# Kernel optimization log

Hardware: AMD Instinct MI355X
Metric: run time of the kernel (lower is better)

## Reference

```python
import jax, jax.numpy as jnp
import numpy as np

N = 100000      # nodes
E = 1600000     # edges (avg degree 16)
D_IN, D_H, D_OUT = 128, 128, 64


def _pow(d, e):
    # torch code zeroes out inf from 0 ** negative_exponent
    p = jnp.power(d, e)
    return jnp.where(jnp.isinf(p), jnp.zeros_like(p), p)


def _gso_weights(params, deg, row, col):
    # params = [m1, m2, m3, e1, e2, e3, a]
    m1, m2, m3, e1, e2, e3, a = (params[i] for i in range(7))
    d = deg + a                       # self-loop-adjusted degrees, [N]
    pe2 = _pow(d, e2)
    pe3 = _pow(d, e3)
    w_edge = m2 * pe2[row] * pe3[col]                     # off-diagonal GSO entries, [E]
    w_self = m1 * _pow(d, e1) + m2 * pe2 * pe3 + m3       # diagonal GSO entries, [N]
    return w_edge, w_self


def setup_inputs() -> dict:
    key = jax.random.key(0)
    ks = jax.random.split(key, 8)
    x = jax.random.normal(ks[0], (N, D_IN), dtype=jnp.float32)
    edge_index = jax.random.randint(ks[1], (2, E), 0, N, dtype=jnp.int32)
    glorot = lambda k, i, o: jax.random.normal(k, (i, o), dtype=jnp.float32) * np.float32(np.sqrt(2.0 / (i + o)))
    W1 = glorot(ks[2], D_IN, D_H)
    W2 = glorot(ks[3], D_H, D_H)
    W3 = glorot(ks[4], D_H, D_OUT)
    b1 = jnp.zeros((D_H,), jnp.float32)
    b2 = jnp.zeros((D_H,), jnp.float32)
    b3 = jnp.zeros((D_OUT,), jnp.float32)
    # [m1, m2, m3, e1, e2, e3, a]
    gso1_params = jnp.array([0.0, 1.0, 0.0, 0.0, -0.5, -0.5, 1.0], jnp.float32)   # NORMADJ
    gso2_params = jnp.array([0.0, -1.0, 1.0, 0.0, -1.0, 0.0, 0.0], jnp.float32)   # RWLAPLACIAN
    return {"x": x, "edge_index": edge_index, "W1": W1, "b1": b1, "W2": W2,
            "b2": b2, "W3": W3, "b3": b3, "gso1_params": gso1_params,
            "gso2_params": gso2_params}


def reference(x, edge_index, W1, b1, W2, b2, W3, b3, gso1_params, gso2_params):
    row, col = edge_index[0], edge_index[1]
    deg = jax.ops.segment_sum(jnp.ones(row.shape, x.dtype), row, num_segments=N)
    we1, ws1 = _gso_weights(gso1_params, deg, row, col)
    we2, ws2 = _gso_weights(gso2_params, deg, row, col)
    w_edge = we1 + we2   # combined two-GSO edge weights, [E]
    w_self = ws1 + ws2   # combined diagonal (self-loop) weights, [N]

    def conv(h, W, b):
        h = h @ W                                                        # [N, d_out]
        agg = jax.ops.segment_sum(w_edge[:, None] * h[col], row, num_segments=N)
        return agg + w_self[:, None] * h + b

    h = jax.nn.relu(conv(x, W1, b1))
    h = jax.nn.relu(conv(h, W2, b2))   # dropout=0.0 (eval) -> identity
    return conv(h, W3, b3)
```

## Files before the change

### kernel.cpp

```cpp
#include <hip/hip_runtime.h>
#include <hip/hip_fp16.h>
#include <math.h>
#include <type_traits>

typedef _Float16 half8 __attribute__((ext_vector_type(8)));
typedef float floatx4 __attribute__((ext_vector_type(4)));

__global__ void deg_count_kernel(const int* __restrict__ row, int* __restrict__ degi, int E) {
    int g = blockIdx.x * blockDim.x + threadIdx.x;
    if (g < E) atomicAdd(&degi[row[g]], 1);
}

__device__ __forceinline__ float pow_z(float d, float e) {
    float p = powf(d, e);
    return isinf(p) ? 0.0f : p;
}

__device__ __forceinline__ void gso_coeff(float deg, const float* __restrict__ p1,
                                          const float* __restrict__ p2,
                                          float4* cf, float* ws) {
    float m1a = p1[0], m2a = p1[1], m3a = p1[2], e1a = p1[3], e2a = p1[4], e3a = p1[5], aa = p1[6];
    float m1b = p2[0], m2b = p2[1], m3b = p2[2], e1b = p2[3], e2b = p2[4], e3b = p2[5], ab = p2[6];
    float d1 = deg + aa, d2 = deg + ab;
    float pa1 = pow_z(d1, e1a), pa2 = pow_z(d1, e2a), pa3 = pow_z(d1, e3a);
    float pb1 = pow_z(d2, e1b), pb2 = pow_z(d2, e2b), pb3 = pow_z(d2, e3b);
    *cf = make_float4(m2a * pa2, pa3, m2b * pb2, pb3);
    *ws = m1a * pa1 + m2a * pa2 * pa3 + m3a
        + m1b * pb1 + m2b * pb2 * pb3 + m3b;
}

__global__ void scan_block_kernel(const int* __restrict__ degi, int* __restrict__ rowptr,
                                  int* __restrict__ blocksum,
                                  const float* __restrict__ p1, const float* __restrict__ p2,
                                  float4* __restrict__ coeff, float* __restrict__ wself, int n) {
    __shared__ int sums[256];
    int tid = threadIdx.x;
    int base = blockIdx.x * 1024 + tid * 4;
    int d0 = (base + 0 < n) ? degi[base + 0] : 0;
    int d1 = (base + 1 < n) ? degi[base + 1] : 0;
    int d2 = (base + 2 < n) ? degi[base + 2] : 0;
    int d3 = (base + 3 < n) ? degi[base + 3] : 0;
    int s0 = d0, s1 = s0 + d1, s2 = s1 + d2, s3 = s2 + d3;
    sums[tid] = s3;
    __syncthreads();
    for (int off = 1; off < 256; off <<= 1) {
        int v = (tid >= off) ? sums[tid - off] : 0;
        __syncthreads();
        sums[tid] += v;
        __syncthreads();
    }
    int excl = sums[tid] - s3;
    if (base + 0 < n) rowptr[base + 1] = excl + s0;
    if (base + 1 < n) rowptr[base + 2] = excl + s1;
    if (base + 2 < n) rowptr[base + 3] = excl + s2;
    if (base + 3 < n) rowptr[base + 4] = excl + s3;
    if (tid == 255) blocksum[blockIdx.x] = sums[255];
    int dd[4] = {d0, d1, d2, d3};
#pragma unroll
    for (int u = 0; u < 4; ++u) {
        if (base + u < n) {
            float4 cf; float ws;
            gso_coeff((float)dd[u], p1, p2, &cf, &ws);
            coeff[base + u] = cf;
            wself[base + u] = ws;
        }
    }
}

__global__ void scan_tops_kernel(const int* __restrict__ blocksum, int* __restrict__ blockoff, int nb) {
    __shared__ int s[128];
    int tid = threadIdx.x;
    int v = (tid < nb) ? blocksum[tid] : 0;
    s[tid] = v;
    __syncthreads();
    for (int off = 1; off < 128; off <<= 1) {
        int u = (tid >= off) ? s[tid - off] : 0;
        __syncthreads();
        s[tid] += u;
        __syncthreads();
    }
    if (tid < nb) blockoff[tid] = s[tid] - v;
}

__global__ void scan_add_kernel(int* __restrict__ rowptr, const int* __restrict__ blockoff, int n) {
    int g = blockIdx.x * blockDim.x + threadIdx.x;
    if (g == 0) rowptr[0] = 0;
    if (g < n) rowptr[g + 1] += blockoff[g >> 10];
}

__global__ __launch_bounds__(256) void partition_kernel(
        const int* __restrict__ row, const int* __restrict__ col,
        const int* __restrict__ rowptr, int* __restrict__ gcur,
        const float4* __restrict__ coeff, int2* __restrict__ epack_mid,
        int E, int shift, int NB) {
    __shared__ int scnt[256], sofs[256], scur[256], gslot[256];
    __shared__ int2 sdata[4096];
    __shared__ unsigned short sbkt[4096];

    int tid = threadIdx.x;
    int base = blockIdx.x * 4096;
    scnt[tid] = 0;
    __syncthreads();

    int epk[16]; float ew[16]; int eb[16];
#pragma unroll
    for (int u = 0; u < 16; ++u) {
        int e = base + u * 256 + tid;
        eb[u] = -1;
        if (e < E) {
            int r = row[e], c = col[e];
            int b = r >> shift;
            eb[u] = b;
            atomicAdd(&scnt[b], 1);
            float4 cr = coeff[r], cc = coeff[c];
            ew[u] = cr.x * cc.y + cr.z * cc.w;
            epk[u] = c | ((r & ((1 << shift) - 1)) << 20);
        }
    }
    __syncthreads();
    sofs[tid] = scnt[tid];
    __syncthreads();
    for (int off = 1; off < 256; off <<= 1) {
        int v = (tid >= off) ? sofs[tid - off] : 0;
        __syncthreads();
        sofs[tid] += v;
        __syncthreads();
    }
    int excl = sofs[tid] - scnt[tid];
    sofs[tid] = excl;
    scur[tid] = excl;
    if (tid < NB && scnt[tid] > 0)
        gslot[tid] = rowptr[tid << shift] + atomicAdd(&gcur[tid], scnt[tid]);
    __syncthreads();
#pragma unroll
    for (int u = 0; u < 16; ++u) {
        if (eb[u] >= 0) {
            int idx = atomicAdd(&scur[eb[u]], 1);
            sdata[idx] = make_int2(epk[u], __float_as_int(ew[u]));
            sbkt[idx] = (unsigned short)eb[u];
        }
    }
    __syncthreads();
    int cntR = min(4096, E - base);
    for (int i = tid; i < cntR; i += 256) {
        int b = sbkt[i];
        epack_mid[gslot[b] + (i - sofs[b])] = sdata[i];
    }
}

__global__ __launch_bounds__(256) void bucket_sort_kernel(
        const int* __restrict__ rowptr, const int2* __restrict__ epack_mid,
        int2* __restrict__ epack, int N, int shift) {
    __shared__ int lcur[4096];
    int b = blockIdx.x;
    int tid = threadIdx.x;
    int rows = 1 << shift;
    int row0 = b << shift;
    for (int j = tid; j < rows; j += 256) {
        int rid = row0 + j;
        if (rid < N) lcur[j] = rowptr[rid];
    }
    __syncthreads();
    int slice0 = rowptr[row0];
    int slice1 = rowptr[min(row0 + rows, N)];
    for (int i = slice0 + tid; i < slice1; i += 256) {
        int2 p = epack_mid[i];
        int rl = ((unsigned)p.x) >> 20;
        int pos = atomicAdd(&lcur[rl], 1);
        epack[pos] = make_int2(p.x & 0xFFFFF, p.y);
    }
}

__global__ void convert_w_all(const float* __restrict__ W1, const float* __restrict__ W2,
                              const float* __restrict__ W3, _Float16* __restrict__ Wt1,
                              _Float16* __restrict__ Wt2, _Float16* __restrict__ Wt3) {
    int g = blockIdx.x * blockDim.x + threadIdx.x;
    if (g < 16384) {
        int k = g >> 7, n = g & 127;
        Wt1[n * 128 + k] = (_Float16)W1[g];
    } else if (g < 32768) {
        int h = g - 16384; int k = h >> 7, n = h & 127;
        Wt2[n * 128 + k] = (_Float16)W2[h];
    } else if (g < 40960) {
        int h = g - 32768; int k = h >> 6, n = h & 63;
        Wt3[n * 128 + k] = (_Float16)W3[h];
    }
}

template<int TN, typename AT>
__global__ __launch_bounds__(256) void gemm_mfma(const AT* __restrict__ A,
        const _Float16* __restrict__ Wt,
        _Float16* __restrict__ C, int n) {
    constexpr int K = 128;
    constexpr int TM = 64;
    constexpr int LDK = K + 8;
    __shared__ _Float16 As[TM][LDK];
    __shared__ _Float16 Bs[TN][LDK];

    int tid = threadIdx.x;
    int wave = tid >> 6, lane = tid & 63;
    int q = lane >> 4, t = lane & 15;
    int rowbase = blockIdx.x * TM;

    if constexpr (std::is_same<AT, float>::value) {
        for (int i = tid; i < TM * K / 4; i += 256) {
            int r = i >> 5;
            int kc = (i & 31) * 4;
            int rr = rowbase + r;
            float4 v = make_float4(0.f, 0.f, 0.f, 0.f);
            if (rr < n) v = *(const float4*)&A[(size_t)rr * K + kc];
            As[r][kc + 0] = (_Float16)v.x;
            As[r][kc + 1] = (_Float16)v.y;
            As[r][kc + 2] = (_Float16)v.z;
            As[r][kc + 3] = (_Float16)v.w;
        }
    } else {
        for (int i = tid; i < TM * K / 8; i += 256) {
            int r = i >> 4;
            int kc = (i & 15) * 8;
            int rr = rowbase + r;
            uint4 v = make_uint4(0u, 0u, 0u, 0u);
            if (rr < n) v = *(const uint4*)&A[(size_t)rr * K + kc];
            *(uint4*)&As[r][kc] = v;
        }
    }
    for (int i = tid; i < TN * K / 8; i += 256) {
        int nr = i >> 4;
        int kc = (i & 15) * 8;
        *(uint4*)&Bs[nr][kc] = *(const uint4*)&Wt[(size_t)nr * K + kc];
    }
    __syncthreads();

    int m0 = wave * 16;
    floatx4 acc[TN / 16];
#pragma unroll
    for (int nt = 0; nt < TN / 16; ++nt) acc[nt] = (floatx4){0.f, 0.f, 0.f, 0.f};

#pragma unroll
    for (int kk = 0; kk < K; kk += 32) {
        half8 a = *(const half8*)&As[m0 + t][kk + q * 8];
#pragma unroll
        for (int nt = 0; nt < TN / 16; ++nt) {
            half8 b = *(const half8*)&Bs[nt * 16 + t][kk + q * 8];
            acc[nt] = __builtin_amdgcn_mfma_f32_16x16x32_f16(a, b, acc[nt], 0, 0, 0);
        }
    }

#pragma unroll
    for (int nt = 0; nt < TN / 16; ++nt) {
#pragma unroll
        for (int r = 0; r < 4; ++r) {
            int rr = rowbase + m0 + q * 4 + r;
            if (rr < n) C[(size_t)rr * TN + nt * 16 + t] = (_Float16)acc[nt][r];
        }
    }
}

__global__ __launch_bounds__(256) void agg128_kernel(const __half2* __restrict__ H,
        const int* __restrict__ rowptr, const int2* __restrict__ epack,
        const float* __restrict__ wself, const float* __restrict__ bias,
        __half2* __restrict__ out, int n) {
    int node = blockIdx.x * 4 + (threadIdx.x >> 6);
    if (node >= n) return;
    int lane = threadIdx.x & 63;
    int start = rowptr[node], end = rowptr[node + 1];
    float ws = wself[node];
    float2 hs = __half22float2(H[(size_t)node * 64 + lane]);
    float ax = ws * hs.x, ay = ws * hs.y;
    int e = start;
    for (; e + 8 <= end; e += 8) {
        int2 p0 = epack[e + 0], p1 = epack[e + 1], p2 = epack[e + 2], p3 = epack[e + 3];
        int2 p4 = epack[e + 4], p5 = epack[e + 5], p6 = epack[e + 6], p7 = epack[e + 7];
        __half2 h0 = H[(size_t)p0.x * 64 + lane];
        __half2 h1 = H[(size_t)p1.x * 64 + lane];
        __half2 h2 = H[(size_t)p2.x * 64 + lane];
        __half2 h3 = H[(size_t)p3.x * 64 + lane];
        __half2 h4 = H[(size_t)p4.x * 64 + lane];
        __half2 h5 = H[(size_t)p5.x * 64 + lane];
        __half2 h6 = H[(size_t)p6.x * 64 + lane];
        __half2 h7 = H[(size_t)p7.x * 64 + lane];
        float2 f0 = __half22float2(h0), f1 = __half22float2(h1);
        float2 f2 = __half22float2(h2), f3 = __half22float2(h3);
        float2 f4 = __half22float2(h4), f5 = __half22float2(h5);
        float2 f6 = __half22float2(h6), f7 = __half22float2(h7);
        float w0 = __int_as_float(p0.y), w1 = __int_as_float(p1.y);
        float w2 = __int_as_float(p2.y), w3 = __int_as_float(p3.y);
        float w4 = __int_as_float(p4.y), w5 = __int_as_float(p5.y);
        float w6 = __int_as_float(p6.y), w7 = __int_as_float(p7.y);
        ax += w0 * f0.x + w1 * f1.x + w2 * f2.x + w3 * f3.x
            + w4 * f4.x + w5 * f5.x + w6 * f6.x + w7 * f7.x;
        ay += w0 * f0.y + w1 * f1.y + w2 * f2.y + w3 * f3.y
            + w4 * f4.y + w5 * f5.y + w6 * f6.y + w7 * f7.y;
    }
    for (; e < end; ++e) {
        int2 pe = epack[e];
        float w = __int_as_float(pe.y);
        float2 f = __half22float2(H[(size_t)pe.x * 64 + lane]);
        ax += w * f.x; ay += w * f.y;
    }
    float2 b = *(const float2*)&bias[2 * lane];
    float vx = fmaxf(ax + b.x, 0.0f);
    float vy = fmaxf(ay + b.y, 0.0f);
    out[(size_t)node * 64 + lane] = __floats2half2_rn(vx, vy);
}

__global__ __launch_bounds__(256) void agg64_kernel(const __half* __restrict__ H,
        const int* __restrict__ rowptr, const int2* __restrict__ epack,
        const float* __restrict__ wself, const float* __restrict__ bias,
        float* __restrict__ out, int n) {
    int node = blockIdx.x * 4 + (threadIdx.x >> 6);
    if (node >= n) return;
    int lane = threadIdx.x & 63;
    int start = rowptr[node], end = rowptr[node + 1];
    float ws = wself[node];
    float acc = ws * __half2float(H[(size_t)node * 64 + lane]);
    int e = start;
    for (; e + 8 <= end; e += 8) {
        int2 p0 = epack[e + 0], p1 = epack[e + 1], p2 = epack[e + 2], p3 = epack[e + 3];
        int2 p4 = epack[e + 4], p5 = epack[e + 5], p6 = epack[e + 6], p7 = epack[e + 7];
        float f0 = __half2float(H[(size_t)p0.x * 64 + lane]);
        float f1 = __half2float(H[(size_t)p1.x * 64 + lane]);
        float f2 = __half2float(H[(size_t)p2.x * 64 + lane]);
        float f3 = __half2float(H[(size_t)p3.x * 64 + lane]);
        float f4 = __half2float(H[(size_t)p4.x * 64 + lane]);
        float f5 = __half2float(H[(size_t)p5.x * 64 + lane]);
        float f6 = __half2float(H[(size_t)p6.x * 64 + lane]);
        float f7 = __half2float(H[(size_t)p7.x * 64 + lane]);
        acc += __int_as_float(p0.y) * f0 + __int_as_float(p1.y) * f1
             + __int_as_float(p2.y) * f2 + __int_as_float(p3.y) * f3
             + __int_as_float(p4.y) * f4 + __int_as_float(p5.y) * f5
             + __int_as_float(p6.y) * f6 + __int_as_float(p7.y) * f7;
    }
    for (; e < end; ++e) {
        int2 pe = epack[e];
        acc += __int_as_float(pe.y) * __half2float(H[(size_t)pe.x * 64 + lane]);
    }
    out[(size_t)node * 64 + lane] = acc + bias[lane];
}

extern "C" void kernel_launch(void* const* d_in, const int* in_sizes, int n_in,
                              void* d_out, int out_size, void* d_ws, size_t ws_size,
                              hipStream_t stream) {
    const float* x  = (const float*)d_in[0];
    const int*   ei = (const int*)d_in[1];
    const float* W1 = (const float*)d_in[2];
    const float* b1 = (const float*)d_in[3];
    const float* W2 = (const float*)d_in[4];
    const float* b2 = (const float*)d_in[5];
    const float* W3 = (const float*)d_in[6];
    const float* b3 = (const float*)d_in[7];
    const float* p1 = (const float*)d_in[8];
    const float* p2 = (const float*)d_in[9];

    const int N = in_sizes[0] / 128;
    const int E = in_sizes[1] / 2;
    const int* row = ei;
    const int* col = ei + E;

    int shift = 0;
    while ((((N - 1) >> shift) + 1) > 256) shift++;
    const int NB = ((N - 1) >> shift) + 1;

    char* p = (char*)d_ws;
    auto alloc = [&](size_t bytes) -> void* {
        void* q = (void*)p;
        p += (bytes + 255) & ~(size_t)255;
        return q;
    };
    int*      degi      = (int*)alloc((size_t)N * 4);
    int*      gcur      = (int*)alloc(256 * 4);
    int*      rowptr    = (int*)alloc((size_t)(N + 1) * 4);
    const int NBLK      = (N + 1023) / 1024;
    int*      blocksum  = (int*)alloc((size_t)NBLK * 4);
    int*      blockoff  = (int*)alloc((size_t)NBLK * 4);
    float4*   coeff     = (float4*)alloc((size_t)N * 16);
    float*    wself     = (float*)alloc((size_t)N * 4);
    int2*     epack_mid = (int2*)alloc((size_t)E * 8);
    int2*     epack     = (int2*)alloc((size_t)E * 8);
    _Float16* Wt1       = (_Float16*)alloc(128 * 128 * 2);
    _Float16* Wt2       = (_Float16*)alloc(128 * 128 * 2);
    _Float16* Wt3       = (_Float16*)alloc(128 * 64 * 2);
    _Float16* bufH      = (_Float16*)alloc((size_t)N * 128 * 2);
    _Float16* actH      = (_Float16*)alloc((size_t)N * 128 * 2);
    (void)ws_size; (void)n_in;

    size_t zero_bytes = (size_t)((char*)rowptr - (char*)degi);
    hipMemsetAsync(degi, 0, zero_bytes, stream);

    convert_w_all<<<160, 256, 0, stream>>>(W1, W2, W3, Wt1, Wt2, Wt3);

    deg_count_kernel<<<(E + 255) / 256, 256, 0, stream>>>(row, degi, E);
    scan_block_kernel<<<NBLK, 256, 0, stream>>>(degi, rowptr, blocksum, p1, p2, coeff, wself, N);
    scan_tops_kernel<<<1, 128, 0, stream>>>(blocksum, blockoff, NBLK);
    scan_add_kernel<<<(N + 255) / 256, 256, 0, stream>>>(rowptr, blockoff, N);
    partition_kernel<<<(E + 4095) / 4096, 256, 0, stream>>>(row, col, rowptr, gcur, coeff,
                                                            epack_mid, E, shift, NB);
    bucket_sort_kernel<<<NB, 256, 0, stream>>>(rowptr, epack_mid, epack, N, shift);

    float* out = (float*)d_out;
    int aggGrid = (N + 3) / 4;
    int gemmGrid = (N + 63) / 64;
    gemm_mfma<128, float><<<gemmGrid, 256, 0, stream>>>(x, Wt1, bufH, N);
    agg128_kernel<<<aggGrid, 256, 0, stream>>>((const __half2*)bufH, rowptr, epack, wself,
                                               b1, (__half2*)actH, N);
    gemm_mfma<128, _Float16><<<gemmGrid, 256, 0, stream>>>(actH, Wt2, bufH, N);
    agg128_kernel<<<aggGrid, 256, 0, stream>>>((const __half2*)bufH, rowptr, epack, wself,
                                               b2, (__half2*)actH, N);
    gemm_mfma<64, _Float16><<<gemmGrid, 256, 0, stream>>>(actH, Wt3, bufH, N);
    agg64_kernel<<<aggGrid, 256, 0, stream>>>((const __half*)bufH, rowptr, epack, wself,
                                              b3, out, N);
}
```

Baseline: 507.2 us.

## Sort edges by row and column chunk, aggregate eight nodes per wave chunk-synchronously

```diff
diff --git a/kernel.cpp b/kernel.cpp
--- a/kernel.cpp
+++ b/kernel.cpp
@@ -6,9 +6,13 @@
 typedef _Float16 half8 __attribute__((ext_vector_type(8)));
 typedef float floatx4 __attribute__((ext_vector_type(4)));
 
-__global__ void deg_count_kernel(const int* __restrict__ row, int* __restrict__ degi, int E) {
+#define CC 16
+#define RSHIFT 9
+
+__global__ void deg_count_kernel(const int* __restrict__ row, const int* __restrict__ col,
+                                 int* __restrict__ degi2, int E, int cshift) {
     int g = blockIdx.x * blockDim.x + threadIdx.x;
-    if (g < E) atomicAdd(&degi[row[g]], 1);
+    if (g < E) atomicAdd(&degi2[row[g] * CC + (col[g] >> cshift)], 1);
 }
 
 __device__ __forceinline__ float pow_z(float d, float e) {
@@ -16,23 +20,24 @@
     return isinf(p) ? 0.0f : p;
 }
 
-__device__ __forceinline__ void gso_coeff(float deg, const float* __restrict__ p1,
-                                          const float* __restrict__ p2,
-                                          float4* cf, float* ws) {
+__global__ void node_coeff_kernel(const int* __restrict__ rowptr2,
+                                  const float* __restrict__ p1, const float* __restrict__ p2,
+                                  float4* __restrict__ coeff, float* __restrict__ wself, int N) {
+    int g = blockIdx.x * blockDim.x + threadIdx.x;
+    if (g >= N) return;
+    float deg = (float)(rowptr2[(size_t)(g + 1) * CC] - rowptr2[(size_t)g * CC]);
     float m1a = p1[0], m2a = p1[1], m3a = p1[2], e1a = p1[3], e2a = p1[4], e3a = p1[5], aa = p1[6];
     float m1b = p2[0], m2b = p2[1], m3b = p2[2], e1b = p2[3], e2b = p2[4], e3b = p2[5], ab = p2[6];
     float d1 = deg + aa, d2 = deg + ab;
     float pa1 = pow_z(d1, e1a), pa2 = pow_z(d1, e2a), pa3 = pow_z(d1, e3a);
     float pb1 = pow_z(d2, e1b), pb2 = pow_z(d2, e2b), pb3 = pow_z(d2, e3b);
-    *cf = make_float4(m2a * pa2, pa3, m2b * pb2, pb3);
-    *ws = m1a * pa1 + m2a * pa2 * pa3 + m3a
-        + m1b * pb1 + m2b * pb2 * pb3 + m3b;
+    coeff[g] = make_float4(m2a * pa2, pa3, m2b * pb2, pb3);
+    wself[g] = m1a * pa1 + m2a * pa2 * pa3 + m3a
+             + m1b * pb1 + m2b * pb2 * pb3 + m3b;
 }
 
 __global__ void scan_block_kernel(const int* __restrict__ degi, int* __restrict__ rowptr,
-                                  int* __restrict__ blocksum,
-                                  const float* __restrict__ p1, const float* __restrict__ p2,
-                                  float4* __restrict__ coeff, float* __restrict__ wself, int n) {
+                                  int* __restrict__ blocksum, int n) {
     __shared__ int sums[256];
     int tid = threadIdx.x;
     int base = blockIdx.x * 1024 + tid * 4;
@@ -55,31 +60,33 @@
     if (base + 2 < n) rowptr[base + 3] = excl + s2;
     if (base + 3 < n) rowptr[base + 4] = excl + s3;
     if (tid == 255) blocksum[blockIdx.x] = sums[255];
-    int dd[4] = {d0, d1, d2, d3};
-#pragma unroll
-    for (int u = 0; u < 4; ++u) {
-        if (base + u < n) {
-            float4 cf; float ws;
-            gso_coeff((float)dd[u], p1, p2, &cf, &ws);
-            coeff[base + u] = cf;
-            wself[base + u] = ws;
-        }
-    }
 }
 
 __global__ void scan_tops_kernel(const int* __restrict__ blocksum, int* __restrict__ blockoff, int nb) {
-    __shared__ int s[128];
+    __shared__ int s[256];
     int tid = threadIdx.x;
-    int v = (tid < nb) ? blocksum[tid] : 0;
-    s[tid] = v;
-    __syncthreads();
-    for (int off = 1; off < 128; off <<= 1) {
-        int u = (tid >= off) ? s[tid - off] : 0;
-        __syncthreads();
-        s[tid] += u;
-        __syncthreads();
-    }
-    if (tid < nb) blockoff[tid] = s[tid] - v;
+    int loc[8]; int tot = 0;
+#pragma unroll
+    for (int u = 0; u < 8; ++u) {
+        int i = tid * 8 + u;
+        loc[u] = (i < nb) ? blocksum[i] : 0;
+        tot += loc[u];
+    }
+    s[tid] = tot;
+    __syncthreads();
+    for (int off = 1; off < 256; off <<= 1) {
+        int v = (tid >= off) ? s[tid - off] : 0;
+        __syncthreads();
+        s[tid] += v;
+        __syncthreads();
+    }
+    int excl = s[tid] - tot;
+#pragma unroll
+    for (int u = 0; u < 8; ++u) {
+        int i = tid * 8 + u;
+        if (i < nb) blockoff[i] = excl;
+        excl += loc[u];
+    }
 }
 
 __global__ void scan_add_kernel(int* __restrict__ rowptr, const int* __restrict__ blockoff, int n) {
@@ -90,9 +97,9 @@
 
 __global__ __launch_bounds__(256) void partition_kernel(
         const int* __restrict__ row, const int* __restrict__ col,
-        const int* __restrict__ rowptr, int* __restrict__ gcur,
+        const int* __restrict__ rowptr2, int* __restrict__ gcur,
         const float4* __restrict__ coeff, int2* __restrict__ epack_mid,
-        int E, int shift, int NB) {
+        int E, int NB) {
     __shared__ int scnt[256], sofs[256], scur[256], gslot[256];
     __shared__ int2 sdata[4096];
     __shared__ unsigned short sbkt[4096];
@@ -109,12 +116,12 @@
         eb[u] = -1;
         if (e < E) {
             int r = row[e], c = col[e];
-            int b = r >> shift;
+            int b = r >> RSHIFT;
             eb[u] = b;
             atomicAdd(&scnt[b], 1);
             float4 cr = coeff[r], cc = coeff[c];
             ew[u] = cr.x * cc.y + cr.z * cc.w;
-            epk[u] = c | ((r & ((1 << shift) - 1)) << 20);
+            epk[u] = c | ((r & ((1 << RSHIFT) - 1)) << 20);
         }
     }
     __syncthreads();
@@ -130,7 +137,7 @@
     sofs[tid] = excl;
     scur[tid] = excl;
     if (tid < NB && scnt[tid] > 0)
-        gslot[tid] = rowptr[tid << shift] + atomicAdd(&gcur[tid], scnt[tid]);
+        gslot[tid] = rowptr2[(size_t)(tid << RSHIFT) * CC] + atomicAdd(&gcur[tid], scnt[tid]);
     __syncthreads();
 #pragma unroll
     for (int u = 0; u < 16; ++u) {
@@ -149,25 +156,26 @@
 }
 
 __global__ __launch_bounds__(256) void bucket_sort_kernel(
-        const int* __restrict__ rowptr, const int2* __restrict__ epack_mid,
-        int2* __restrict__ epack, int N, int shift) {
-    __shared__ int lcur[4096];
+        const int* __restrict__ rowptr2, const int2* __restrict__ epack_mid,
+        int2* __restrict__ epack, int N, int cshift) {
+    __shared__ int lcur[(1 << RSHIFT) * CC];
     int b = blockIdx.x;
     int tid = threadIdx.x;
-    int rows = 1 << shift;
-    int row0 = b << shift;
-    for (int j = tid; j < rows; j += 256) {
-        int rid = row0 + j;
-        if (rid < N) lcur[j] = rowptr[rid];
-    }
-    __syncthreads();
-    int slice0 = rowptr[row0];
-    int slice1 = rowptr[min(row0 + rows, N)];
+    int rows = 1 << RSHIFT;
+    int row0 = b << RSHIFT;
+    int nslots = (min(rows, N - row0)) * CC;
+    for (int j = tid; j < nslots; j += 256)
+        lcur[j] = rowptr2[(size_t)row0 * CC + j];
+    __syncthreads();
+    int slice0 = rowptr2[(size_t)row0 * CC];
+    int slice1 = rowptr2[(size_t)min(row0 + rows, N) * CC];
     for (int i = slice0 + tid; i < slice1; i += 256) {
         int2 p = epack_mid[i];
+        int colv = p.x & 0xFFFFF;
         int rl = ((unsigned)p.x) >> 20;
-        int pos = atomicAdd(&lcur[rl], 1);
-        epack[pos] = make_int2(p.x & 0xFFFFF, p.y);
+        int ch = colv >> cshift;
+        int pos = atomicAdd(&lcur[rl * CC + ch], 1);
+        epack[pos] = make_int2(colv, p.y);
     }
 }
 
@@ -189,8 +197,7 @@
 
 template<int TN, typename AT>
 __global__ __launch_bounds__(256) void gemm_mfma(const AT* __restrict__ A,
-        const _Float16* __restrict__ Wt,
-        _Float16* __restrict__ C, int n) {
+        const _Float16* __restrict__ Wt, _Float16* __restrict__ C, int n) {
     constexpr int K = 128;
     constexpr int TM = 64;
     constexpr int LDK = K + 8;
@@ -257,85 +264,114 @@
 }
 
 __global__ __launch_bounds__(256) void agg128_kernel(const __half2* __restrict__ H,
-        const int* __restrict__ rowptr, const int2* __restrict__ epack,
+        const int* __restrict__ rowptr2, const int2* __restrict__ epack,
         const float* __restrict__ wself, const float* __restrict__ bias,
-        __half2* __restrict__ out, int n) {
-    int node = blockIdx.x * 4 + (threadIdx.x >> 6);
-    if (node >= n) return;
-    int lane = threadIdx.x & 63;
-    int start = rowptr[node], end = rowptr[node + 1];
-    float ws = wself[node];
-    float2 hs = __half22float2(H[(size_t)node * 64 + lane]);
-    float ax = ws * hs.x, ay = ws * hs.y;
-    int e = start;
-    for (; e + 8 <= end; e += 8) {
-        int2 p0 = epack[e + 0], p1 = epack[e + 1], p2 = epack[e + 2], p3 = epack[e + 3];
-        int2 p4 = epack[e + 4], p5 = epack[e + 5], p6 = epack[e + 6], p7 = epack[e + 7];
-        __half2 h0 = H[(size_t)p0.x * 64 + lane];
-        __half2 h1 = H[(size_t)p1.x * 64 + lane];
-        __half2 h2 = H[(size_t)p2.x * 64 + lane];
-        __half2 h3 = H[(size_t)p3.x * 64 + lane];
-        __half2 h4 = H[(size_t)p4.x * 64 + lane];
-        __half2 h5 = H[(size_t)p5.x * 64 + lane];
-        __half2 h6 = H[(size_t)p6.x * 64 + lane];
-        __half2 h7 = H[(size_t)p7.x * 64 + lane];
-        float2 f0 = __half22float2(h0), f1 = __half22float2(h1);
-        float2 f2 = __half22float2(h2), f3 = __half22float2(h3);
-        float2 f4 = __half22float2(h4), f5 = __half22float2(h5);
-        float2 f6 = __half22float2(h6), f7 = __half22float2(h7);
-        float w0 = __int_as_float(p0.y), w1 = __int_as_float(p1.y);
-        float w2 = __int_as_float(p2.y), w3 = __int_as_float(p3.y);
-        float w4 = __int_as_float(p4.y), w5 = __int_as_float(p5.y);
-        float w6 = __int_as_float(p6.y), w7 = __int_as_float(p7.y);
-        ax += w0 * f0.x + w1 * f1.x + w2 * f2.x + w3 * f3.x
-            + w4 * f4.x + w5 * f5.x + w6 * f6.x + w7 * f7.x;
-        ay += w0 * f0.y + w1 * f1.y + w2 * f2.y + w3 * f3.y
-            + w4 * f4.y + w5 * f5.y + w6 * f6.y + w7 * f7.y;
-    }
-    for (; e < end; ++e) {
-        int2 pe = epack[e];
-        float w = __int_as_float(pe.y);
-        float2 f = __half22float2(H[(size_t)pe.x * 64 + lane]);
-        ax += w * f.x; ay += w * f.y;
+        __half2* __restrict__ out, int n, int nchunk) {
+    int wave = threadIdx.x >> 6, lane = threadIdx.x & 63;
+    int node0 = blockIdx.x * 32 + wave * 8;
+    if (node0 >= n) return;
+    int nv = min(8, n - node0);
+    float ax[8], ay[8];
+#pragma unroll
+    for (int i = 0; i < 8; ++i) { ax[i] = 0.f; ay[i] = 0.f; }
+#pragma unroll
+    for (int i = 0; i < 8; ++i) {
+        if (i < nv) {
+            float w = wself[node0 + i];
+            float2 h = __half22float2(H[(size_t)(node0 + i) * 64 + lane]);
+            ax[i] = w * h.x; ay[i] = w * h.y;
+        }
+    }
+    for (int c = 0; c < nchunk; ++c) {
+        int sa[8], ea[8];
+#pragma unroll
+        for (int i = 0; i < 8; ++i) {
+            sa[i] = (i < nv) ? rowptr2[(size_t)(node0 + i) * CC + c] : 0;
+            ea[i] = (i < nv) ? rowptr2[(size_t)(node0 + i) * CC + c + 1] : 0;
+        }
+        for (;;) {
+            bool any = false;
+            int2 pk[8];
+#pragma unroll
+            for (int i = 0; i < 8; ++i) {
+                if (sa[i] < ea[i]) { pk[i] = epack[sa[i]]; any = true; }
+            }
+            if (!any) break;
+            __half2 hh[8];
+#pragma unroll
+            for (int i = 0; i < 8; ++i)
+                if (sa[i] < ea[i]) hh[i] = H[(size_t)pk[i].x * 64 + lane];
+#pragma unroll
+            for (int i = 0; i < 8; ++i) {
+                if (sa[i] < ea[i]) {
+                    float w = __int_as_float(pk[i].y);
+                    float2 f = __half22float2(hh[i]);
+                    ax[i] += w * f.x; ay[i] += w * f.y;
+                    sa[i]++;
+                }
+            }
+        }
     }
     float2 b = *(const float2*)&bias[2 * lane];
-    float vx = fmaxf(ax + b.x, 0.0f);
-    float vy = fmaxf(ay + b.y, 0.0f);
-    out[(size_t)node * 64 + lane] = __floats2half2_rn(vx, vy);
+#pragma unroll
+    for (int i = 0; i < 8; ++i) {
+        if (i < nv) {
+            float vx = fmaxf(ax[i] + b.x, 0.f);
+            float vy = fmaxf(ay[i] + b.y, 0.f);
+            out[(size_t)(node0 + i) * 64 + lane] = __floats2half2_rn(vx, vy);
+        }
+    }
 }
 
 __global__ __launch_bounds__(256) void agg64_kernel(const __half* __restrict__ H,
-        const int* __restrict__ rowptr, const int2* __restrict__ epack,
+        const int* __restrict__ rowptr2, const int2* __restrict__ epack,
         const float* __restrict__ wself, const float* __restrict__ bias,
-        float* __restrict__ out, int n) {
-    int node = blockIdx.x * 4 + (threadIdx.x >> 6);
-    if (node >= n) return;
-    int lane = threadIdx.x & 63;
-    int start = rowptr[node], end = rowptr[node + 1];
-    float ws = wself[node];
-    float acc = ws * __half2float(H[(size_t)node * 64 + lane]);
-    int e = start;
-    for (; e + 8 <= end; e += 8) {
-        int2 p0 = epack[e + 0], p1 = epack[e + 1], p2 = epack[e + 2], p3 = epack[e + 3];
-        int2 p4 = epack[e + 4], p5 = epack[e + 5], p6 = epack[e + 6], p7 = epack[e + 7];
-        float f0 = __half2float(H[(size_t)p0.x * 64 + lane]);
-        float f1 = __half2float(H[(size_t)p1.x * 64 + lane]);
-        float f2 = __half2float(H[(size_t)p2.x * 64 + lane]);
-        float f3 = __half2float(H[(size_t)p3.x * 64 + lane]);
-        float f4 = __half2float(H[(size_t)p4.x * 64 + lane]);
-        float f5 = __half2float(H[(size_t)p5.x * 64 + lane]);
-        float f6 = __half2float(H[(size_t)p6.x * 64 + lane]);
-        float f7 = __half2float(H[(size_t)p7.x * 64 + lane]);
-        acc += __int_as_float(p0.y) * f0 + __int_as_float(p1.y) * f1
-             + __int_as_float(p2.y) * f2 + __int_as_float(p3.y) * f3
-             + __int_as_float(p4.y) * f4 + __int_as_float(p5.y) * f5
-             + __int_as_float(p6.y) * f6 + __int_as_float(p7.y) * f7;
-    }
-    for (; e < end; ++e) {
-        int2 pe = epack[e];
-        acc += __int_as_float(pe.y) * __half2float(H[(size_t)pe.x * 64 + lane]);
-    }
-    out[(size_t)node * 64 + lane] = acc + bias[lane];
+        float* __restrict__ out, int n, int nchunk) {
+    int wave = threadIdx.x >> 6, lane = threadIdx.x & 63;
+    int node0 = blockIdx.x * 32 + wave * 8;
+    if (node0 >= n) return;
+    int nv = min(8, n - node0);
+    float acc[8];
+#pragma unroll
+    for (int i = 0; i < 8; ++i) acc[i] = 0.f;
+#pragma unroll
+    for (int i = 0; i < 8; ++i) {
+        if (i < nv)
+            acc[i] = wself[node0 + i] * __half2float(H[(size_t)(node0 + i) * 64 + lane]);
+    }
+    for (int c = 0; c < nchunk; ++c) {
+        int sa[8], ea[8];
+#pragma unroll
+        for (int i = 0; i < 8; ++i) {
+            sa[i] = (i < nv) ? rowptr2[(size_t)(node0 + i) * CC + c] : 0;
+            ea[i] = (i < nv) ? rowptr2[(size_t)(node0 + i) * CC + c + 1] : 0;
+        }
+        for (;;) {
+            bool any = false;
+            int2 pk[8];
+#pragma unroll
+            for (int i = 0; i < 8; ++i) {
+                if (sa[i] < ea[i]) { pk[i] = epack[sa[i]]; any = true; }
+            }
+            if (!any) break;
+            float f[8];
+#pragma unroll
+            for (int i = 0; i < 8; ++i)
+                if (sa[i] < ea[i]) f[i] = __half2float(H[(size_t)pk[i].x * 64 + lane]);
+#pragma unroll
+            for (int i = 0; i < 8; ++i) {
+                if (sa[i] < ea[i]) {
+                    acc[i] += __int_as_float(pk[i].y) * f[i];
+                    sa[i]++;
+                }
+            }
+        }
+    }
+    float b = bias[lane];
+#pragma unroll
+    for (int i = 0; i < 8; ++i) {
+        if (i < nv) out[(size_t)(node0 + i) * 64 + lane] = acc[i] + b;
+    }
 }
 
 extern "C" void kernel_launch(void* const* d_in, const int* in_sizes, int n_in,
@@ -357,9 +393,11 @@
     const int* row = ei;
     const int* col = ei + E;
 
-    int shift = 0;
-    while ((((N - 1) >> shift) + 1) > 256) shift++;
-    const int NB = ((N - 1) >> shift) + 1;
+    int cshift = 0;
+    while (((N - 1) >> cshift) > (CC - 1)) cshift++;
+    const int nchunk = ((N - 1) >> cshift) + 1;
+    const int NB = ((N - 1) >> RSHIFT) + 1;
+    const int n2 = N * CC;
 
     char* p = (char*)d_ws;
     auto alloc = [&](size_t bytes) -> void* {
@@ -367,10 +405,10 @@
         p += (bytes + 255) & ~(size_t)255;
         return q;
     };
-    int*      degi      = (int*)alloc((size_t)N * 4);
+    int*      degi2     = (int*)alloc((size_t)n2 * 4);
     int*      gcur      = (int*)alloc(256 * 4);
-    int*      rowptr    = (int*)alloc((size_t)(N + 1) * 4);
-    const int NBLK      = (N + 1023) / 1024;
+    int*      rowptr2   = (int*)alloc((size_t)(n2 + 1) * 4);
+    const int NBLK      = (n2 + 1023) / 1024;
     int*      blocksum  = (int*)alloc((size_t)NBLK * 4);
     int*      blockoff  = (int*)alloc((size_t)NBLK * 4);
     float4*   coeff     = (float4*)alloc((size_t)N * 16);
@@ -384,29 +422,30 @@
     _Float16* actH      = (_Float16*)alloc((size_t)N * 128 * 2);
     (void)ws_size; (void)n_in;
 
-    size_t zero_bytes = (size_t)((char*)rowptr - (char*)degi);
-    hipMemsetAsync(degi, 0, zero_bytes, stream);
+    size_t zero_bytes = (size_t)((char*)rowptr2 - (char*)degi2);
+    hipMemsetAsync(degi2, 0, zero_bytes, stream);
 
     convert_w_all<<<160, 256, 0, stream>>>(W1, W2, W3, Wt1, Wt2, Wt3);
 
-    deg_count_kernel<<<(E + 255) / 256, 256, 0, stream>>>(row, degi, E);
-    scan_block_kernel<<<NBLK, 256, 0, stream>>>(degi, rowptr, blocksum, p1, p2, coeff, wself, N);
-    scan_tops_kernel<<<1, 128, 0, stream>>>(blocksum, blockoff, NBLK);
-    scan_add_kernel<<<(N + 255) / 256, 256, 0, stream>>>(rowptr, blockoff, N);
-    partition_kernel<<<(E + 4095) / 4096, 256, 0, stream>>>(row, col, rowptr, gcur, coeff,
-                                                            epack_mid, E, shift, NB);
-    bucket_sort_kernel<<<NB, 256, 0, stream>>>(rowptr, epack_mid, epack, N, shift);
+    deg_count_kernel<<<(E + 255) / 256, 256, 0, stream>>>(row, col, degi2, E, cshift);
+    scan_block_kernel<<<NBLK, 256, 0, stream>>>(degi2, rowptr2, blocksum, n2);
+    scan_tops_kernel<<<1, 256, 0, stream>>>(blocksum, blockoff, NBLK);
+    scan_add_kernel<<<(n2 + 255) / 256, 256, 0, stream>>>(rowptr2, blockoff, n2);
+    node_coeff_kernel<<<(N + 255) / 256, 256, 0, stream>>>(rowptr2, p1, p2, coeff, wself, N);
+    partition_kernel<<<(E + 4095) / 4096, 256, 0, stream>>>(row, col, rowptr2, gcur, coeff,
+                                                            epack_mid, E, NB);
+    bucket_sort_kernel<<<NB, 256, 0, stream>>>(rowptr2, epack_mid, epack, N, cshift);
 
     float* out = (float*)d_out;
-    int aggGrid = (N + 3) / 4;
+    int aggGrid = (N + 31) / 32;
     int gemmGrid = (N + 63) / 64;
     gemm_mfma<128, float><<<gemmGrid, 256, 0, stream>>>(x, Wt1, bufH, N);
-    agg128_kernel<<<aggGrid, 256, 0, stream>>>((const __half2*)bufH, rowptr, epack, wself,
-                                               b1, (__half2*)actH, N);
+    agg128_kernel<<<aggGrid, 256, 0, stream>>>((const __half2*)bufH, rowptr2, epack, wself,
+                                               b1, (__half2*)actH, N, nchunk);
     gemm_mfma<128, _Float16><<<gemmGrid, 256, 0, stream>>>(actH, Wt2, bufH, N);
-    agg128_kernel<<<aggGrid, 256, 0, stream>>>((const __half2*)bufH, rowptr, epack, wself,
-                                               b2, (__half2*)actH, N);
+    agg128_kernel<<<aggGrid, 256, 0, stream>>>((const __half2*)bufH, rowptr2, epack, wself,
+                                               b2, (__half2*)actH, N, nchunk);
     gemm_mfma<64, _Float16><<<gemmGrid, 256, 0, stream>>>(actH, Wt3, bufH, N);
-    agg64_kernel<<<aggGrid, 256, 0, stream>>>((const __half*)bufH, rowptr, epack, wself,
-                                              b3, out, N);
-}
+    agg64_kernel<<<aggGrid, 256, 0, stream>>>((const __half*)bufH, rowptr2, epack, wself,
+                                              b3, out, N, nchunk);
+}
```

New measurement: 955.0 us. +88.3%, slower.

## Enlarge GEMM row tile and software-pipeline edge index loads in aggregation

Applied to the files above, without the earlier changes.

```diff
diff --git a/kernel.cpp b/kernel.cpp
--- a/kernel.cpp
+++ b/kernel.cpp
@@ -189,10 +189,9 @@
 
 template<int TN, typename AT>
 __global__ __launch_bounds__(256) void gemm_mfma(const AT* __restrict__ A,
-        const _Float16* __restrict__ Wt,
-        _Float16* __restrict__ C, int n) {
+        const _Float16* __restrict__ Wt, _Float16* __restrict__ C, int n) {
     constexpr int K = 128;
-    constexpr int TM = 64;
+    constexpr int TM = 128;
     constexpr int LDK = K + 8;
     __shared__ _Float16 As[TM][LDK];
     __shared__ _Float16 Bs[TN][LDK];
@@ -231,18 +230,23 @@
     }
     __syncthreads();
 
-    int m0 = wave * 16;
-    floatx4 acc[TN / 16];
-#pragma unroll
-    for (int nt = 0; nt < TN / 16; ++nt) acc[nt] = (floatx4){0.f, 0.f, 0.f, 0.f};
+    int m0 = wave * 32;
+    floatx4 acc0[TN / 16], acc1[TN / 16];
+#pragma unroll
+    for (int nt = 0; nt < TN / 16; ++nt) {
+        acc0[nt] = (floatx4){0.f, 0.f, 0.f, 0.f};
+        acc1[nt] = (floatx4){0.f, 0.f, 0.f, 0.f};
+    }
 
 #pragma unroll
     for (int kk = 0; kk < K; kk += 32) {
-        half8 a = *(const half8*)&As[m0 + t][kk + q * 8];
+        half8 a0 = *(const half8*)&As[m0 + t][kk + q * 8];
+        half8 a1 = *(const half8*)&As[m0 + 16 + t][kk + q * 8];
 #pragma unroll
         for (int nt = 0; nt < TN / 16; ++nt) {
             half8 b = *(const half8*)&Bs[nt * 16 + t][kk + q * 8];
-            acc[nt] = __builtin_amdgcn_mfma_f32_16x16x32_f16(a, b, acc[nt], 0, 0, 0);
+            acc0[nt] = __builtin_amdgcn_mfma_f32_16x16x32_f16(a0, b, acc0[nt], 0, 0, 0);
+            acc1[nt] = __builtin_amdgcn_mfma_f32_16x16x32_f16(a1, b, acc1[nt], 0, 0, 0);
         }
     }
 
@@ -250,8 +254,10 @@
     for (int nt = 0; nt < TN / 16; ++nt) {
 #pragma unroll
         for (int r = 0; r < 4; ++r) {
-            int rr = rowbase + m0 + q * 4 + r;
-            if (rr < n) C[(size_t)rr * TN + nt * 16 + t] = (_Float16)acc[nt][r];
+            int rr0 = rowbase + m0 + q * 4 + r;
+            if (rr0 < n) C[(size_t)rr0 * TN + nt * 16 + t] = (_Float16)acc0[nt][r];
+            int rr1 = rr0 + 16;
+            if (rr1 < n) C[(size_t)rr1 * TN + nt * 16 + t] = (_Float16)acc1[nt][r];
         }
     }
 }
@@ -267,36 +273,33 @@
     float ws = wself[node];
     float2 hs = __half22float2(H[(size_t)node * 64 + lane]);
     float ax = ws * hs.x, ay = ws * hs.y;
-    int e = start;
-    for (; e + 8 <= end; e += 8) {
-        int2 p0 = epack[e + 0], p1 = epack[e + 1], p2 = epack[e + 2], p3 = epack[e + 3];
-        int2 p4 = epack[e + 4], p5 = epack[e + 5], p6 = epack[e + 6], p7 = epack[e + 7];
-        __half2 h0 = H[(size_t)p0.x * 64 + lane];
-        __half2 h1 = H[(size_t)p1.x * 64 + lane];
-        __half2 h2 = H[(size_t)p2.x * 64 + lane];
-        __half2 h3 = H[(size_t)p3.x * 64 + lane];
-        __half2 h4 = H[(size_t)p4.x * 64 + lane];
-        __half2 h5 = H[(size_t)p5.x * 64 + lane];
-        __half2 h6 = H[(size_t)p6.x * 64 + lane];
-        __half2 h7 = H[(size_t)p7.x * 64 + lane];
-        float2 f0 = __half22float2(h0), f1 = __half22float2(h1);
-        float2 f2 = __half22float2(h2), f3 = __half22float2(h3);
-        float2 f4 = __half22float2(h4), f5 = __half22float2(h5);
-        float2 f6 = __half22float2(h6), f7 = __half22float2(h7);
-        float w0 = __int_as_float(p0.y), w1 = __int_as_float(p1.y);
-        float w2 = __int_as_float(p2.y), w3 = __int_as_float(p3.y);
-        float w4 = __int_as_float(p4.y), w5 = __int_as_float(p5.y);
-        float w6 = __int_as_float(p6.y), w7 = __int_as_float(p7.y);
-        ax += w0 * f0.x + w1 * f1.x + w2 * f2.x + w3 * f3.x
-            + w4 * f4.x + w5 * f5.x + w6 * f6.x + w7 * f7.x;
-        ay += w0 * f0.y + w1 * f1.y + w2 * f2.y + w3 * f3.y
-            + w4 * f4.y + w5 * f5.y + w6 * f6.y + w7 * f7.y;
-    }
-    for (; e < end; ++e) {
-        int2 pe = epack[e];
-        float w = __int_as_float(pe.y);
-        float2 f = __half22float2(H[(size_t)pe.x * 64 + lane]);
-        ax += w * f.x; ay += w * f.y;
+    if (start < end) {
+        int last = end - 1;
+        int2 p[8];
+#pragma unroll
+        for (int j = 0; j < 8; ++j) p[j] = epack[min(start + j, last)];
+        for (int e = start; e < end; e += 8) {
+            int en = e + 8;
+            bool more = en < end;
+            int2 pn[8];
+            if (more) {
+#pragma unroll
+                for (int j = 0; j < 8; ++j) pn[j] = epack[min(en + j, last)];
+            }
+            __half2 hh[8];
+#pragma unroll
+            for (int j = 0; j < 8; ++j) hh[j] = H[(size_t)p[j].x * 64 + lane];
+#pragma unroll
+            for (int j = 0; j < 8; ++j) {
+                float w = (e + j < end) ? __int_as_float(p[j].y) : 0.f;
+                float2 f = __half22float2(hh[j]);
+                ax += w * f.x; ay += w * f.y;
+            }
+            if (more) {
+#pragma unroll
+                for (int j = 0; j < 8; ++j) p[j] = pn[j];
+            }
+        }
     }
     float2 b = *(const float2*)&bias[2 * lane];
     float vx = fmaxf(ax + b.x, 0.0f);
@@ -314,26 +317,32 @@
     int start = rowptr[node], end = rowptr[node + 1];
     float ws = wself[node];
     float acc = ws * __half2float(H[(size_t)node * 64 + lane]);
-    int e = start;
-    for (; e + 8 <= end; e += 8) {
-        int2 p0 = epack[e + 0], p1 = epack[e + 1], p2 = epack[e + 2], p3 = epack[e + 3];
-        int2 p4 = epack[e + 4], p5 = epack[e + 5], p6 = epack[e + 6], p7 = epack[e + 7];
-        float f0 = __half2float(H[(size_t)p0.x * 64 + lane]);
-        float f1 = __half2float(H[(size_t)p1.x * 64 + lane]);
-        float f2 = __half2float(H[(size_t)p2.x * 64 + lane]);
-        float f3 = __half2float(H[(size_t)p3.x * 64 + lane]);
-        float f4 = __half2float(H[(size_t)p4.x * 64 + lane]);
-        float f5 = __half2float(H[(size_t)p5.x * 64 + lane]);
-        float f6 = __half2float(H[(size_t)p6.x * 64 + lane]);
-        float f7 = __half2float(H[(size_t)p7.x * 64 + lane]);
-        acc += __int_as_float(p0.y) * f0 + __int_as_float(p1.y) * f1
-             + __int_as_float(p2.y) * f2 + __int_as_float(p3.y) * f3
-             + __int_as_float(p4.y) * f4 + __int_as_float(p5.y) * f5
-             + __int_as_float(p6.y) * f6 + __int_as_float(p7.y) * f7;
-    }
-    for (; e < end; ++e) {
-        int2 pe = epack[e];
-        acc += __int_as_float(pe.y) * __half2float(H[(size_t)pe.x * 64 + lane]);
+    if (start < end) {
+        int last = end - 1;
+        int2 p[8];
+#pragma unroll
+        for (int j = 0; j < 8; ++j) p[j] = epack[min(start + j, last)];
+        for (int e = start; e < end; e += 8) {
+            int en = e + 8;
+            bool more = en < end;
+            int2 pn[8];
+            if (more) {
+#pragma unroll
+                for (int j = 0; j < 8; ++j) pn[j] = epack[min(en + j, last)];
+            }
+            float f[8];
+#pragma unroll
+            for (int j = 0; j < 8; ++j) f[j] = __half2float(H[(size_t)p[j].x * 64 + lane]);
+#pragma unroll
+            for (int j = 0; j < 8; ++j) {
+                float w = (e + j < end) ? __int_as_float(p[j].y) : 0.f;
+                acc += w * f[j];
+            }
+            if (more) {
+#pragma unroll
+                for (int j = 0; j < 8; ++j) p[j] = pn[j];
+            }
+        }
     }
     out[(size_t)node * 64 + lane] = acc + bias[lane];
 }
@@ -399,7 +408,7 @@
 
     float* out = (float*)d_out;
     int aggGrid = (N + 3) / 4;
-    int gemmGrid = (N + 63) / 64;
+    int gemmGrid = (N + 127) / 128;
     gemm_mfma<128, float><<<gemmGrid, 256, 0, stream>>>(x, Wt1, bufH, N);
     agg128_kernel<<<aggGrid, 256, 0, stream>>>((const __half2*)bufH, rowptr, epack, wself,
                                                b1, (__half2*)actH, N);
```

Measured after the change: 535.1 us. +5.5%, slower.
